# Kernel tuning notes

Measured on AMD Instinct MI355X. Metric: run time of the kernel, lower is better.

The kernel has to match this reference:

```python
import jax, jax.numpy as jnp
import numpy as np

N = 50000      # nodes
E = 800000     # edges
T_MAX = 128
N_T = 128
NF = T_MAX * 3 # 384 node features


def setup_inputs() -> dict:
    key = jax.random.key(0)
    ks = jax.random.split(key, 12)
    def lin(k, fi, fo):
        k1, k2 = jax.random.split(k)
        s = 1.0 / np.sqrt(fi)
        return (jax.random.uniform(k1, (fi, fo), jnp.float32, -s, s),
                jax.random.uniform(k2, (fo,), jnp.float32, -s, s))
    x = jax.random.normal(ks[0], (N, NF), jnp.float32)
    edge_index = jax.random.randint(ks[1], (2, E), 0, N, jnp.int32)
    W1, b1 = lin(ks[2], NF, N_T)
    W2, b2 = lin(ks[3], N_T, N_T * 3)
    W3, b3 = lin(ks[4], N_T * 3, N_T * 2)
    W4, b4 = lin(ks[5], N_T * 2, NF)
    Wl, bl = lin(ks[6], NF, T_MAX)
    return {"x": x, "edge_index": edge_index,
            "W1": W1, "b1": b1, "W2": W2, "b2": b2,
            "W3": W3, "b3": b3, "W4": W4, "b4": b4,
            "Wl": Wl, "bl": bl}


def reference(x, edge_index, W1, b1, W2, b2, W3, b3, W4, b4, Wl, bl):
    # GCNConv (PyG defaults): add self-loops, symmetric normalization
    loop = jnp.arange(N, dtype=edge_index.dtype)
    src = jnp.concatenate([edge_index[0], loop])
    dst = jnp.concatenate([edge_index[1], loop])
    deg = jax.ops.segment_sum(jnp.ones_like(src, jnp.float32), dst, num_segments=N)
    dinv = jax.lax.rsqrt(deg)  # deg >= 1 due to self-loops
    norm = (dinv[src] * dinv[dst])[:, None]  # [E+N, 1]

    def gcn(h, W, b):
        hw = h @ W                       # [N, out]
        msg = hw[src] * norm             # gather + scale per edge
        agg = jax.ops.segment_sum(msg, dst, num_segments=N)
        return agg + b

    # dropout is identity in eval mode
    h = jax.nn.leaky_relu(gcn(x, W1, b1))
    h = jax.nn.leaky_relu(gcn(h, W2, b2))
    h = jax.nn.leaky_relu(gcn(h, W3, b3))
    h = jax.nn.leaky_relu(gcn(h, W4, b4))
    h = h @ Wl + bl
    return jax.nn.relu(h)  # args.schedule_deviation == False
```

## Files before the change

kernel.cpp:

```cpp
#include <hip/hip_runtime.h>

#define NNODES 50000
#define NEDGES 800000
#define NTILES ((NNODES + 255) / 256)

typedef unsigned short ushort_t;
typedef __attribute__((ext_vector_type(8))) short short8;
typedef __attribute__((ext_vector_type(4))) float floatx4;

__device__ __forceinline__ float bf2f(unsigned short u) {
  union { unsigned int i; float f; } v; v.i = ((unsigned int)u) << 16; return v.f;
}
__device__ __forceinline__ unsigned short f2bf(float f) {
  union { float f; unsigned int i; } v; v.f = f;
  unsigned int r = v.i + 0x7fffu + ((v.i >> 16) & 1u);
  return (unsigned short)(r >> 16);
}

__device__ __forceinline__ void gload_lds16(const void* g, void* l) {
  __builtin_amdgcn_global_load_lds(
      (const __attribute__((address_space(1))) unsigned int*)g,
      (__attribute__((address_space(3))) unsigned int*)l, 16, 0, 0);
}


__global__ void hist_kernel(const int* dst, int* cnt) {
  int i = blockIdx.x * 256 + threadIdx.x;
  if (i < NEDGES) atomicAdd(&cnt[dst[i]], 1);
}

__global__ void dinv_kernel(const int* cnt, float* dinv) {
  int i = blockIdx.x * 256 + threadIdx.x;
  if (i < NNODES) dinv[i] = rsqrtf((float)(cnt[i] + 1));
}


__global__ __launch_bounds__(256) void tile_scan_kernel(
    const int* __restrict__ cnt, int* __restrict__ tile_pref, int* __restrict__ tile_sum) {
  __shared__ int s[256];
  int b = blockIdx.x, t = threadIdx.x;
  int i = b * 256 + t;
  int v = (i < NNODES) ? cnt[i] : 0;
  s[t] = v;
  __syncthreads();
#pragma unroll
  for (int off = 1; off < 256; off <<= 1) {
    int x = (t >= off) ? s[t - off] : 0;
    __syncthreads();
    s[t] += x;
    __syncthreads();
  }
  if (i < NNODES) tile_pref[i] = s[t] - v;
  if (t == 255) tile_sum[b] = s[255];
}

__global__ __launch_bounds__(256) void sum_scan_kernel(
    const int* __restrict__ tile_sum, int* __restrict__ tile_base) {
  __shared__ int s[256];
  int t = threadIdx.x;
  int v = (t < NTILES) ? tile_sum[t] : 0;
  s[t] = v;
  __syncthreads();
#pragma unroll
  for (int off = 1; off < 256; off <<= 1) {
    int x = (t >= off) ? s[t - off] : 0;
    __syncthreads();
    s[t] += x;
    __syncthreads();
  }
  if (t < NTILES) tile_base[t] = s[t] - v;
}

__global__ __launch_bounds__(256) void scan_write_kernel(
    const int* __restrict__ cnt, const int* __restrict__ tile_pref,
    const int* __restrict__ tile_base, int* __restrict__ row_ptr,
    int* __restrict__ cursor) {
  int b = blockIdx.x, t = threadIdx.x;
  int i = b * 256 + t;
  if (i < NNODES) {
    int base = tile_base[b] + tile_pref[i];
    row_ptr[i] = base;
    cursor[i] = base;
    if (i == NNODES - 1) row_ptr[NNODES] = base + cnt[i];
  }
}

__global__ void fill_kernel(const int* src, const int* dst, int* cursor, int* col_idx) {
  int i = blockIdx.x * 256 + threadIdx.x;
  if (i < NEDGES) {
    int p = atomicAdd(&cursor[dst[i]], 1);
    col_idx[p] = src[i];
  }
}

__global__ void wprep_kernel(const float* W, ushort_t* hi, ushort_t* lo, int K, int N) {
  int idx = blockIdx.x * 256 + threadIdx.x;
  if (idx < K * N) {
    int n = idx / K, k = idx - n * K;
    float w = W[(size_t)k * N + n];
    unsigned short h = f2bf(w);
    hi[idx] = h;
    lo[idx] = f2bf(w - bf2f(h));
  }
}


template <int WPL>
__device__ __forceinline__ void load_row(const ushort_t* p, float* f) {
  if (WPL == 2) {
    unsigned int u = *(const unsigned int*)p;
    f[0] = bf2f((unsigned short)(u & 0xffff));
    f[1] = bf2f((unsigned short)(u >> 16));
  } else {
    uint2 u = *(const uint2*)p;
    f[0] = bf2f((unsigned short)(u.x & 0xffff));
    f[1] = bf2f((unsigned short)(u.x >> 16));
    f[2] = bf2f((unsigned short)(u.y & 0xffff));
    f[3] = bf2f((unsigned short)(u.y >> 16));
  }
}

template <int WPL>
__global__ __launch_bounds__(256) void agg_kernel(
    const ushort_t* __restrict__ in, ushort_t* __restrict__ out,
    const int* __restrict__ row_ptr, const int* __restrict__ col_idx,
    const float* __restrict__ dinv, const float* __restrict__ bias,
    int mode, int scale_store) {
  const int W = WPL * 64;
  int wid = blockIdx.x * 4 + (threadIdx.x >> 6);
  int lane = threadIdx.x & 63;
  int co = lane * WPL;
  const ushort_t* base = in + co;
  float acc[WPL];
  {
    float v[WPL];
    load_row<WPL>(base + (size_t)wid * W, v);
#pragma unroll
    for (int c = 0; c < WPL; ++c) acc[c] = v[c];
  }
  int e = row_ptr[wid], e1 = row_ptr[wid + 1];
  for (; e + 16 <= e1; e += 16) {
    int j[16];
#pragma unroll
    for (int q = 0; q < 16; ++q) j[q] = col_idx[e + q];
    float v[16][WPL];
#pragma unroll
    for (int q = 0; q < 16; ++q) load_row<WPL>(base + (size_t)j[q] * W, v[q]);
#pragma unroll
    for (int c = 0; c < WPL; ++c) {
      float s0 = (v[0][c] + v[1][c]) + (v[2][c] + v[3][c]);
      float s1 = (v[4][c] + v[5][c]) + (v[6][c] + v[7][c]);
      float s2 = (v[8][c] + v[9][c]) + (v[10][c] + v[11][c]);
      float s3 = (v[12][c] + v[13][c]) + (v[14][c] + v[15][c]);
      acc[c] += (s0 + s1) + (s2 + s3);
    }
  }
  for (; e + 4 <= e1; e += 4) {
    int j0 = col_idx[e], j1 = col_idx[e + 1], j2 = col_idx[e + 2], j3 = col_idx[e + 3];
    float v0[WPL], v1[WPL], v2[WPL], v3[WPL];
    load_row<WPL>(base + (size_t)j0 * W, v0);
    load_row<WPL>(base + (size_t)j1 * W, v1);
    load_row<WPL>(base + (size_t)j2 * W, v2);
    load_row<WPL>(base + (size_t)j3 * W, v3);
#pragma unroll
    for (int c = 0; c < WPL; ++c) acc[c] += (v0[c] + v1[c]) + (v2[c] + v3[c]);
  }
  for (; e < e1; ++e) {
    int j = col_idx[e];
    float v[WPL];
    load_row<WPL>(base + (size_t)j * W, v);
#pragma unroll
    for (int c = 0; c < WPL; ++c) acc[c] += v[c];
  }
  float di = dinv[wid];
  unsigned short o[WPL];
  if (mode) {
    float bb[WPL];
    if constexpr (WPL == 2) {
      float2 b2 = *(const float2*)(bias + co); bb[0] = b2.x; bb[1] = b2.y;
    } else {
      float4 b4 = *(const float4*)(bias + co);
      bb[0] = b4.x; bb[1] = b4.y; bb[2] = b4.z; bb[3] = b4.w;
    }
    float sc = scale_store ? di : 1.f;
#pragma unroll
    for (int c = 0; c < WPL; ++c) {
      float v = acc[c] * di + bb[c];
      v = v > 0.f ? v : 0.01f * v;
      o[c] = f2bf(v * sc);
    }
  } else {
#pragma unroll
    for (int c = 0; c < WPL; ++c) o[c] = f2bf(acc[c] * di);
  }
  if constexpr (WPL == 2) {
    *(unsigned int*)(out + (size_t)wid * W + co) =
        (unsigned int)o[0] | ((unsigned int)o[1] << 16);
  } else {
    uint2 u;
    u.x = (unsigned int)o[0] | ((unsigned int)o[1] << 16);
    u.y = (unsigned int)o[2] | ((unsigned int)o[3] << 16);
    *(uint2*)(out + (size_t)wid * W + co) = u;
  }
}


#define BK 32

template <int TBM, int TBN>
__global__ __launch_bounds__(256, TBM == 64 ? 6 : 4) void gemm_mfma(
    const void* __restrict__ Av, const ushort_t* __restrict__ Bhi,
    const ushort_t* __restrict__ Blo, void* __restrict__ Cv,
    const float* __restrict__ bias, const float* __restrict__ dinv,
    int M, int K, int ldc, int mode, int scale_store, int out_f32, int a_f32) {
  constexpr int FR = TBM / 32;
  constexpr int FG = TBN / 32;
  constexpr int AIT = TBM / 64;
  constexpr int BIT = TBN / 64;
  __shared__ ushort_t As[TBM * BK];
  __shared__ ushort_t Bh[TBN * BK];
  __shared__ ushort_t Bl[TBN * BK];
  int tid = threadIdx.x;
  int lane = tid & 63, w = tid >> 6;
  int wm = w & 1, wn = w >> 1;
  int m0 = blockIdx.x * TBM, n0 = blockIdx.y * TBN;
  floatx4 acc[FR][FG] = {};
  int nkt = K / BK;
  for (int kt = 0; kt < nkt; ++kt) {
    int kb = kt * BK;
    uint4 va[AIT];
    if (a_f32) {
      const float* Af = (const float*)Av;
#pragma unroll
      for (int it = 0; it < AIT; ++it) {
        int s = it * 256 + tid;
        int row = s >> 2, ks = (s & 3) * 8;
        int gr = m0 + row; if (gr > M - 1) gr = M - 1;
        float4 p0 = *(const float4*)(Af + (size_t)gr * K + kb + ks);
        float4 p1 = *(const float4*)(Af + (size_t)gr * K + kb + ks + 4);
        uint4 u;
        u.x = (unsigned int)f2bf(p0.x) | ((unsigned int)f2bf(p0.y) << 16);
        u.y = (unsigned int)f2bf(p0.z) | ((unsigned int)f2bf(p0.w) << 16);
        u.z = (unsigned int)f2bf(p1.x) | ((unsigned int)f2bf(p1.y) << 16);
        u.w = (unsigned int)f2bf(p1.z) | ((unsigned int)f2bf(p1.w) << 16);
        va[it] = u;
      }
    }
    __syncthreads();
    if (a_f32) {
#pragma unroll
      for (int it = 0; it < AIT; ++it) {
        int s = it * 256 + tid;
        *(uint4*)&As[s * 8] = va[it];
      }
    } else {
#pragma unroll
      for (int it = 0; it < AIT; ++it) {
        int s = it * 256 + tid;
        int row = s >> 2, ks = (s & 3) * 8;
        int gr = m0 + row; if (gr > M - 1) gr = M - 1;
        gload_lds16((const ushort_t*)Av + (size_t)gr * K + kb + ks,
                    As + (size_t)(it * 256 + w * 64) * 8);
      }
    }
#pragma unroll
    for (int it = 0; it < BIT; ++it) {
      int s = it * 256 + tid;
      int row = s >> 2, ks = (s & 3) * 8;
      gload_lds16(Bhi + (size_t)(n0 + row) * K + kb + ks,
                  Bh + (size_t)(it * 256 + w * 64) * 8);
      gload_lds16(Blo + (size_t)(n0 + row) * K + kb + ks,
                  Bl + (size_t)(it * 256 + w * 64) * 8);
    }
    __syncthreads();
    short8 af[FR], fh[FG], fl[FG];
#pragma unroll
    for (int f = 0; f < FR; ++f)
      af[f] = *(const short8*)&As[(wm * (TBM / 2) + f * 16 + (lane & 15)) * BK + (lane >> 4) * 8];
#pragma unroll
    for (int g = 0; g < FG; ++g) {
      int o = (wn * (TBN / 2) + g * 16 + (lane & 15)) * BK + (lane >> 4) * 8;
      fh[g] = *(const short8*)&Bh[o];
      fl[g] = *(const short8*)&Bl[o];
    }
#pragma unroll
    for (int f = 0; f < FR; ++f)
#pragma unroll
      for (int g = 0; g < FG; ++g) {
        acc[f][g] = __builtin_amdgcn_mfma_f32_16x16x32_bf16(af[f], fh[g], acc[f][g], 0, 0, 0);
        acc[f][g] = __builtin_amdgcn_mfma_f32_16x16x32_bf16(af[f], fl[g], acc[f][g], 0, 0, 0);
      }
  }
  int cr = lane >> 4, cc = lane & 15;
#pragma unroll
  for (int f = 0; f < FR; ++f) {
#pragma unroll
    for (int r = 0; r < 4; ++r) {
      int row = m0 + wm * (TBM / 2) + f * 16 + cr * 4 + r;
      if (row >= M) continue;
      float sc = scale_store ? dinv[row] : 1.f;
#pragma unroll
      for (int g = 0; g < FG; ++g) {
        int col = n0 + wn * (TBN / 2) + g * 16 + cc;
        float v = acc[f][g][r];
        if (mode) {
          v += bias[col];
          v = (mode == 1) ? (v > 0.f ? v : 0.01f * v) : (v > 0.f ? v : 0.f);
        }
        v *= sc;
        if (out_f32) ((float*)Cv)[(size_t)row * ldc + col] = v;
        else ((ushort_t*)Cv)[(size_t)row * ldc + col] = f2bf(v);
      }
    }
  }
}


extern "C" void kernel_launch(void* const* d_in, const int* in_sizes, int n_in,
                              void* d_out, int out_size, void* d_ws, size_t ws_size,
                              hipStream_t stream) {
  const float* x  = (const float*)d_in[0];
  const int* ei   = (const int*)d_in[1];
  const float* W1 = (const float*)d_in[2];
  const float* b1 = (const float*)d_in[3];
  const float* W2 = (const float*)d_in[4];
  const float* b2 = (const float*)d_in[5];
  const float* W3 = (const float*)d_in[6];
  const float* b3 = (const float*)d_in[7];
  const float* W4 = (const float*)d_in[8];
  const float* b4 = (const float*)d_in[9];
  const float* Wl = (const float*)d_in[10];
  const float* bl = (const float*)d_in[11];

  char* p = (char*)d_ws;
  auto alloc = [&](size_t bytes) {
    char* r = p;
    p += (bytes + 255) & ~(size_t)255;
    return r;
  };
  int* cnt       = (int*)alloc((size_t)NNODES * 4);
  int* cursor    = (int*)alloc((size_t)NNODES * 4);
  int* row_ptr   = (int*)alloc((size_t)(NNODES + 1) * 4);
  float* dinv    = (float*)alloc((size_t)NNODES * 4);
  int* col_idx   = (int*)alloc((size_t)NEDGES * 4);
  int* tile_pref = (int*)alloc((size_t)NNODES * 4);
  int* tile_sum  = (int*)alloc(256 * 4);
  int* tile_base = (int*)alloc(256 * 4);
  ushort_t* W1h = (ushort_t*)alloc(49152 * 2); ushort_t* W1l = (ushort_t*)alloc(49152 * 2);
  ushort_t* W2h = (ushort_t*)alloc(49152 * 2); ushort_t* W2l = (ushort_t*)alloc(49152 * 2);
  ushort_t* W3h = (ushort_t*)alloc(98304 * 2); ushort_t* W3l = (ushort_t*)alloc(98304 * 2);
  ushort_t* W4h = (ushort_t*)alloc(98304 * 2); ushort_t* W4l = (ushort_t*)alloc(98304 * 2);
  ushort_t* Wlh = (ushort_t*)alloc(49152 * 2); ushort_t* Wll = (ushort_t*)alloc(49152 * 2);
  ushort_t* actA = (ushort_t*)alloc((size_t)NNODES * 384 * 2);
  ushort_t* actB = (ushort_t*)alloc((size_t)NNODES * 384 * 2);

  const int* src = ei;
  const int* dst = ei + NEDGES;

  hipMemsetAsync(cnt, 0, (size_t)NNODES * 4, stream);
  hist_kernel<<<(NEDGES + 255) / 256, 256, 0, stream>>>(dst, cnt);
  tile_scan_kernel<<<NTILES, 256, 0, stream>>>(cnt, tile_pref, tile_sum);
  sum_scan_kernel<<<1, 256, 0, stream>>>(tile_sum, tile_base);
  scan_write_kernel<<<NTILES, 256, 0, stream>>>(cnt, tile_pref, tile_base, row_ptr, cursor);
  dinv_kernel<<<(NNODES + 255) / 256, 256, 0, stream>>>(cnt, dinv);
  fill_kernel<<<(NEDGES + 255) / 256, 256, 0, stream>>>(src, dst, cursor, col_idx);

  wprep_kernel<<<(49152 + 255) / 256, 256, 0, stream>>>(W1, W1h, W1l, 384, 128);
  wprep_kernel<<<(49152 + 255) / 256, 256, 0, stream>>>(W2, W2h, W2l, 128, 384);
  wprep_kernel<<<(98304 + 255) / 256, 256, 0, stream>>>(W3, W3h, W3l, 384, 256);
  wprep_kernel<<<(98304 + 255) / 256, 256, 0, stream>>>(W4, W4h, W4l, 256, 384);
  wprep_kernel<<<(49152 + 255) / 256, 256, 0, stream>>>(Wl, Wlh, Wll, 384, 128);

  dim3 blk(256);
  int gm64  = (NNODES + 63) / 64;
  int gm128 = (NNODES + 127) / 128;
  int nagg = NNODES / 4;

  gemm_mfma<64, 64><<<dim3(gm64, 2), blk, 0, stream>>>(x, W1h, W1l, actA, (const float*)0, dinv, NNODES, 384, 128, 0, 1, 0, 1);
  agg_kernel<2><<<nagg, blk, 0, stream>>>(actA, actB, row_ptr, col_idx, dinv, b1, 1, 1);
  agg_kernel<2><<<nagg, blk, 0, stream>>>(actB, actA, row_ptr, col_idx, dinv, (const float*)0, 0, 0);
  gemm_mfma<128, 128><<<dim3(gm128, 3), blk, 0, stream>>>(actA, W2h, W2l, actB, b2, dinv, NNODES, 128, 384, 1, 0, 0, 0);
  gemm_mfma<128, 128><<<dim3(gm128, 2), blk, 0, stream>>>(actB, W3h, W3l, actA, (const float*)0, dinv, NNODES, 384, 256, 0, 1, 0, 0);
  agg_kernel<4><<<nagg, blk, 0, stream>>>(actA, actB, row_ptr, col_idx, dinv, b3, 1, 1);
  agg_kernel<4><<<nagg, blk, 0, stream>>>(actB, actA, row_ptr, col_idx, dinv, (const float*)0, 0, 0);
  gemm_mfma<128, 128><<<dim3(gm128, 3), blk, 0, stream>>>(actA, W4h, W4l, actB, b4, dinv, NNODES, 256, 384, 1, 0, 0, 0);
  gemm_mfma<64, 64><<<dim3(gm64, 2), blk, 0, stream>>>(actB, Wlh, Wll, d_out, bl, dinv, NNODES, 384, 128, 2, 0, 1, 0);
}
```

Baseline: 612.9 us.

## Store aggregation inputs in 32-column chunked layout and gather per chunk

GEMM outputs feeding the aggregation are now written in a column-chunked layout, 32 columns per chunk stored contiguously across nodes. A new aggregation kernel gathers one chunk per grid-y slice with 16 threads per node, so each gathered neighbour row is a 64-byte contiguous segment. The aim is a smaller per-chunk working set that stays in cache during random neighbour gathers, traded against more redundant col_idx reads and scattered 2-byte GEMM stores. It also fuses dinv into the scan-write kernel and the five weight-prep launches into one.

```diff
diff --git a/kernel.cpp b/kernel.cpp
--- a/kernel.cpp
+++ b/kernel.cpp
@@ -28,12 +28,6 @@
   int i = blockIdx.x * 256 + threadIdx.x;
   if (i < NEDGES) atomicAdd(&cnt[dst[i]], 1);
 }
-
-__global__ void dinv_kernel(const int* cnt, float* dinv) {
-  int i = blockIdx.x * 256 + threadIdx.x;
-  if (i < NNODES) dinv[i] = rsqrtf((float)(cnt[i] + 1));
-}
-
 
 __global__ __launch_bounds__(256) void tile_scan_kernel(
     const int* __restrict__ cnt, int* __restrict__ tile_pref, int* __restrict__ tile_sum) {
@@ -74,13 +68,14 @@
 __global__ __launch_bounds__(256) void scan_write_kernel(
     const int* __restrict__ cnt, const int* __restrict__ tile_pref,
     const int* __restrict__ tile_base, int* __restrict__ row_ptr,
-    int* __restrict__ cursor) {
+    int* __restrict__ cursor, float* __restrict__ dinv) {
   int b = blockIdx.x, t = threadIdx.x;
   int i = b * 256 + t;
   if (i < NNODES) {
     int base = tile_base[b] + tile_pref[i];
     row_ptr[i] = base;
     cursor[i] = base;
+    dinv[i] = rsqrtf((float)(cnt[i] + 1));
     if (i == NNODES - 1) row_ptr[NNODES] = base + cnt[i];
   }
 }
@@ -93,115 +88,78 @@
   }
 }
 
-__global__ void wprep_kernel(const float* W, ushort_t* hi, ushort_t* lo, int K, int N) {
+__global__ void wprep_all(
+    const float* __restrict__ W1, const float* __restrict__ W2,
+    const float* __restrict__ W3, const float* __restrict__ W4,
+    const float* __restrict__ Wl,
+    ushort_t* W1h, ushort_t* W1l, ushort_t* W2h, ushort_t* W2l,
+    ushort_t* W3h, ushort_t* W3l, ushort_t* W4h, ushort_t* W4l,
+    ushort_t* Wlh, ushort_t* Wll) {
   int idx = blockIdx.x * 256 + threadIdx.x;
-  if (idx < K * N) {
-    int n = idx / K, k = idx - n * K;
-    float w = W[(size_t)k * N + n];
-    unsigned short h = f2bf(w);
-    hi[idx] = h;
-    lo[idx] = f2bf(w - bf2f(h));
-  }
-}
-
-
-template <int WPL>
-__device__ __forceinline__ void load_row(const ushort_t* p, float* f) {
-  if (WPL == 2) {
-    unsigned int u = *(const unsigned int*)p;
-    f[0] = bf2f((unsigned short)(u & 0xffff));
-    f[1] = bf2f((unsigned short)(u >> 16));
-  } else {
-    uint2 u = *(const uint2*)p;
-    f[0] = bf2f((unsigned short)(u.x & 0xffff));
-    f[1] = bf2f((unsigned short)(u.x >> 16));
-    f[2] = bf2f((unsigned short)(u.y & 0xffff));
-    f[3] = bf2f((unsigned short)(u.y >> 16));
-  }
-}
-
-template <int WPL>
-__global__ __launch_bounds__(256) void agg_kernel(
+  const float* W; ushort_t* ph; ushort_t* pl; int K, N, base;
+  if (idx < 49152)       { W = W1; ph = W1h; pl = W1l; K = 384; N = 128; base = 0; }
+  else if (idx < 98304)  { W = W2; ph = W2h; pl = W2l; K = 128; N = 384; base = 49152; }
+  else if (idx < 196608) { W = W3; ph = W3h; pl = W3l; K = 384; N = 256; base = 98304; }
+  else if (idx < 294912) { W = W4; ph = W4h; pl = W4l; K = 256; N = 384; base = 196608; }
+  else if (idx < 344064) { W = Wl; ph = Wlh; pl = Wll; K = 384; N = 128; base = 294912; }
+  else return;
+  int i = idx - base;
+  int n = i / K, k = i - n * K;
+  float w = W[(size_t)k * N + n];
+  unsigned short h = f2bf(w);
+  ph[i] = h;
+  pl[i] = f2bf(w - bf2f(h));
+}
+
+__global__ __launch_bounds__(256) void agg_chunked(
     const ushort_t* __restrict__ in, ushort_t* __restrict__ out,
     const int* __restrict__ row_ptr, const int* __restrict__ col_idx,
     const float* __restrict__ dinv, const float* __restrict__ bias,
-    int mode, int scale_store) {
-  const int W = WPL * 64;
-  int wid = blockIdx.x * 4 + (threadIdx.x >> 6);
-  int lane = threadIdx.x & 63;
-  int co = lane * WPL;
-  const ushort_t* base = in + co;
-  float acc[WPL];
-  {
-    float v[WPL];
-    load_row<WPL>(base + (size_t)wid * W, v);
-#pragma unroll
-    for (int c = 0; c < WPL; ++c) acc[c] = v[c];
-  }
-  int e = row_ptr[wid], e1 = row_ptr[wid + 1];
-  for (; e + 16 <= e1; e += 16) {
-    int j[16];
-#pragma unroll
-    for (int q = 0; q < 16; ++q) j[q] = col_idx[e + q];
-    float v[16][WPL];
-#pragma unroll
-    for (int q = 0; q < 16; ++q) load_row<WPL>(base + (size_t)j[q] * W, v[q]);
-#pragma unroll
-    for (int c = 0; c < WPL; ++c) {
-      float s0 = (v[0][c] + v[1][c]) + (v[2][c] + v[3][c]);
-      float s1 = (v[4][c] + v[5][c]) + (v[6][c] + v[7][c]);
-      float s2 = (v[8][c] + v[9][c]) + (v[10][c] + v[11][c]);
-      float s3 = (v[12][c] + v[13][c]) + (v[14][c] + v[15][c]);
-      acc[c] += (s0 + s1) + (s2 + s3);
-    }
-  }
-  for (; e + 4 <= e1; e += 4) {
-    int j0 = col_idx[e], j1 = col_idx[e + 1], j2 = col_idx[e + 2], j3 = col_idx[e + 3];
-    float v0[WPL], v1[WPL], v2[WPL], v3[WPL];
-    load_row<WPL>(base + (size_t)j0 * W, v0);
-    load_row<WPL>(base + (size_t)j1 * W, v1);
-    load_row<WPL>(base + (size_t)j2 * W, v2);
-    load_row<WPL>(base + (size_t)j3 * W, v3);
-#pragma unroll
-    for (int c = 0; c < WPL; ++c) acc[c] += (v0[c] + v1[c]) + (v2[c] + v3[c]);
+    int W, int mode, int scale_store, int out_chunked) {
+  int t = threadIdx.x;
+  int node = blockIdx.x * 16 + (t >> 4);
+  if (node >= NNODES) return;
+  int cp = t & 15;
+  int chunk = blockIdx.y;
+  int col = chunk * 32 + cp * 2;
+  const ushort_t* cbase = in + (size_t)chunk * NNODES * 32 + cp * 2;
+  unsigned int u = *(const unsigned int*)(cbase + (size_t)node * 32);
+  float a0 = bf2f((unsigned short)(u & 0xffff));
+  float a1 = bf2f((unsigned short)(u >> 16));
+  int e = row_ptr[node], e1 = row_ptr[node + 1];
+  for (; e + 8 <= e1; e += 8) {
+    unsigned int uu[8];
+#pragma unroll
+    for (int q = 0; q < 8; ++q) {
+      int j = col_idx[e + q];
+      uu[q] = *(const unsigned int*)(cbase + (size_t)j * 32);
+    }
+#pragma unroll
+    for (int q = 0; q < 8; ++q) {
+      a0 += bf2f((unsigned short)(uu[q] & 0xffff));
+      a1 += bf2f((unsigned short)(uu[q] >> 16));
+    }
   }
   for (; e < e1; ++e) {
     int j = col_idx[e];
-    float v[WPL];
-    load_row<WPL>(base + (size_t)j * W, v);
-#pragma unroll
-    for (int c = 0; c < WPL; ++c) acc[c] += v[c];
-  }
-  float di = dinv[wid];
-  unsigned short o[WPL];
+    unsigned int uu = *(const unsigned int*)(cbase + (size_t)j * 32);
+    a0 += bf2f((unsigned short)(uu & 0xffff));
+    a1 += bf2f((unsigned short)(uu >> 16));
+  }
+  float di = dinv[node];
+  a0 *= di; a1 *= di;
   if (mode) {
-    float bb[WPL];
-    if constexpr (WPL == 2) {
-      float2 b2 = *(const float2*)(bias + co); bb[0] = b2.x; bb[1] = b2.y;
-    } else {
-      float4 b4 = *(const float4*)(bias + co);
-      bb[0] = b4.x; bb[1] = b4.y; bb[2] = b4.z; bb[3] = b4.w;
-    }
-    float sc = scale_store ? di : 1.f;
-#pragma unroll
-    for (int c = 0; c < WPL; ++c) {
-      float v = acc[c] * di + bb[c];
-      v = v > 0.f ? v : 0.01f * v;
-      o[c] = f2bf(v * sc);
-    }
-  } else {
-#pragma unroll
-    for (int c = 0; c < WPL; ++c) o[c] = f2bf(acc[c] * di);
-  }
-  if constexpr (WPL == 2) {
-    *(unsigned int*)(out + (size_t)wid * W + co) =
-        (unsigned int)o[0] | ((unsigned int)o[1] << 16);
-  } else {
-    uint2 u;
-    u.x = (unsigned int)o[0] | ((unsigned int)o[1] << 16);
-    u.y = (unsigned int)o[2] | ((unsigned int)o[3] << 16);
-    *(uint2*)(out + (size_t)wid * W + co) = u;
-  }
+    float2 bb = *(const float2*)(bias + col);
+    a0 += bb.x; a1 += bb.y;
+    a0 = a0 > 0.f ? a0 : 0.01f * a0;
+    a1 = a1 > 0.f ? a1 : 0.01f * a1;
+    if (scale_store) { a0 *= di; a1 *= di; }
+  }
+  unsigned int o = (unsigned int)f2bf(a0) | ((unsigned int)f2bf(a1) << 16);
+  if (out_chunked)
+    *(unsigned int*)(out + (size_t)chunk * NNODES * 32 + (size_t)node * 32 + cp * 2) = o;
+  else
+    *(unsigned int*)(out + (size_t)node * W + col) = o;
 }
 
 
@@ -212,7 +170,7 @@
     const void* __restrict__ Av, const ushort_t* __restrict__ Bhi,
     const ushort_t* __restrict__ Blo, void* __restrict__ Cv,
     const float* __restrict__ bias, const float* __restrict__ dinv,
-    int M, int K, int ldc, int mode, int scale_store, int out_f32, int a_f32) {
+    int M, int K, int ldc, int mode, int scale_store, int out_mode, int a_f32) {
   constexpr int FR = TBM / 32;
   constexpr int FG = TBN / 32;
   constexpr int AIT = TBM / 64;
@@ -308,7 +266,9 @@
           v = (mode == 1) ? (v > 0.f ? v : 0.01f * v) : (v > 0.f ? v : 0.f);
         }
         v *= sc;
-        if (out_f32) ((float*)Cv)[(size_t)row * ldc + col] = v;
+        if (out_mode == 1) ((float*)Cv)[(size_t)row * ldc + col] = v;
+        else if (out_mode == 2)
+          ((ushort_t*)Cv)[((size_t)(col >> 5) * NNODES + row) * 32 + (col & 31)] = f2bf(v);
         else ((ushort_t*)Cv)[(size_t)row * ldc + col] = f2bf(v);
       }
     }
@@ -361,28 +321,23 @@
   hist_kernel<<<(NEDGES + 255) / 256, 256, 0, stream>>>(dst, cnt);
   tile_scan_kernel<<<NTILES, 256, 0, stream>>>(cnt, tile_pref, tile_sum);
   sum_scan_kernel<<<1, 256, 0, stream>>>(tile_sum, tile_base);
-  scan_write_kernel<<<NTILES, 256, 0, stream>>>(cnt, tile_pref, tile_base, row_ptr, cursor);
-  dinv_kernel<<<(NNODES + 255) / 256, 256, 0, stream>>>(cnt, dinv);
+  scan_write_kernel<<<NTILES, 256, 0, stream>>>(cnt, tile_pref, tile_base, row_ptr, cursor, dinv);
   fill_kernel<<<(NEDGES + 255) / 256, 256, 0, stream>>>(src, dst, cursor, col_idx);
-
-  wprep_kernel<<<(49152 + 255) / 256, 256, 0, stream>>>(W1, W1h, W1l, 384, 128);
-  wprep_kernel<<<(49152 + 255) / 256, 256, 0, stream>>>(W2, W2h, W2l, 128, 384);
-  wprep_kernel<<<(98304 + 255) / 256, 256, 0, stream>>>(W3, W3h, W3l, 384, 256);
-  wprep_kernel<<<(98304 + 255) / 256, 256, 0, stream>>>(W4, W4h, W4l, 256, 384);
-  wprep_kernel<<<(49152 + 255) / 256, 256, 0, stream>>>(Wl, Wlh, Wll, 384, 128);
+  wprep_all<<<(344064 + 255) / 256, 256, 0, stream>>>(
+      W1, W2, W3, W4, Wl, W1h, W1l, W2h, W2l, W3h, W3l, W4h, W4l, Wlh, Wll);
 
   dim3 blk(256);
   int gm64  = (NNODES + 63) / 64;
   int gm128 = (NNODES + 127) / 128;
-  int nagg = NNODES / 4;
-
-  gemm_mfma<64, 64><<<dim3(gm64, 2), blk, 0, stream>>>(x, W1h, W1l, actA, (const float*)0, dinv, NNODES, 384, 128, 0, 1, 0, 1);
-  agg_kernel<2><<<nagg, blk, 0, stream>>>(actA, actB, row_ptr, col_idx, dinv, b1, 1, 1);
-  agg_kernel<2><<<nagg, blk, 0, stream>>>(actB, actA, row_ptr, col_idx, dinv, (const float*)0, 0, 0);
+  int gagg  = NNODES / 16;
+
+  gemm_mfma<64, 64><<<dim3(gm64, 2), blk, 0, stream>>>(x, W1h, W1l, actA, (const float*)0, dinv, NNODES, 384, 128, 0, 1, 2, 1);
+  agg_chunked<<<dim3(gagg, 4), blk, 0, stream>>>(actA, actB, row_ptr, col_idx, dinv, b1, 128, 1, 1, 1);
+  agg_chunked<<<dim3(gagg, 4), blk, 0, stream>>>(actB, actA, row_ptr, col_idx, dinv, (const float*)0, 128, 0, 0, 0);
   gemm_mfma<128, 128><<<dim3(gm128, 3), blk, 0, stream>>>(actA, W2h, W2l, actB, b2, dinv, NNODES, 128, 384, 1, 0, 0, 0);
-  gemm_mfma<128, 128><<<dim3(gm128, 2), blk, 0, stream>>>(actB, W3h, W3l, actA, (const float*)0, dinv, NNODES, 384, 256, 0, 1, 0, 0);
-  agg_kernel<4><<<nagg, blk, 0, stream>>>(actA, actB, row_ptr, col_idx, dinv, b3, 1, 1);
-  agg_kernel<4><<<nagg, blk, 0, stream>>>(actB, actA, row_ptr, col_idx, dinv, (const float*)0, 0, 0);
+  gemm_mfma<128, 128><<<dim3(gm128, 2), blk, 0, stream>>>(actB, W3h, W3l, actA, (const float*)0, dinv, NNODES, 384, 256, 0, 1, 2, 0);
+  agg_chunked<<<dim3(gagg, 8), blk, 0, stream>>>(actA, actB, row_ptr, col_idx, dinv, b3, 256, 1, 1, 1);
+  agg_chunked<<<dim3(gagg, 8), blk, 0, stream>>>(actB, actA, row_ptr, col_idx, dinv, (const float*)0, 256, 0, 0, 0);
   gemm_mfma<128, 128><<<dim3(gm128, 3), blk, 0, stream>>>(actA, W4h, W4l, actB, b4, dinv, NNODES, 256, 384, 1, 0, 0, 0);
   gemm_mfma<64, 64><<<dim3(gm64, 2), blk, 0, stream>>>(actB, Wlh, Wll, d_out, bl, dinv, NNODES, 384, 128, 2, 0, 1, 0);
 }
```

After: 696.0 us. +13.6%, slower.
